# Optimization experiments

Measured on AMD Instinct MI355X. Metric: run time of the kernel, lower is better.

## Reference

```python
import jax, jax.numpy as jnp
import numpy as np

B, S, HID = 1, 2048, 2048
NH, NKV, HD = 32, 8, 64
SCALE = HD ** -0.5


def _rotary_tables(seq_len, dim, base=10000.0):
    inv_freq = 1.0 / (base ** (jnp.arange(0, dim, 2, dtype=jnp.float32) / dim))
    t = jnp.arange(seq_len, dtype=jnp.float32)
    freqs = jnp.outer(t, inv_freq)                      # [S, D/2]
    emb = jnp.concatenate([freqs, freqs], axis=-1)      # [S, D]
    return jnp.cos(emb)[None], jnp.sin(emb)[None]       # [1, S, D]


def setup_inputs() -> dict:
    key = jax.random.key(0)
    ks = jax.random.split(key, 5)
    cos, sin = _rotary_tables(S, HD)
    std = HID ** -0.5
    return {
        "hidden_states": jax.random.normal(ks[0], (B, S, HID), jnp.float32),
        "cos": cos,
        "sin": sin,
        "Wq": jax.random.normal(ks[1], (HID, NH * HD), jnp.float32) * std,
        "Wk": jax.random.normal(ks[2], (HID, NKV * HD), jnp.float32) * std,
        "Wv": jax.random.normal(ks[3], (HID, NKV * HD), jnp.float32) * std,
        "Wo": jax.random.normal(ks[4], (NH * HD, HID), jnp.float32) * std,
    }


def _rotate_half(x):
    x1, x2 = jnp.split(x, 2, axis=-1)
    return jnp.concatenate([-x2, x1], axis=-1)


def reference(hidden_states, cos, sin, Wq, Wk, Wv, Wo):
    b, s, _ = hidden_states.shape
    # projections -> [B, H, S, D]
    q = (hidden_states @ Wq).reshape(b, s, NH, HD).transpose(0, 2, 1, 3)
    k = (hidden_states @ Wk).reshape(b, s, NKV, HD).transpose(0, 2, 1, 3)
    v = (hidden_states @ Wv).reshape(b, s, NKV, HD).transpose(0, 2, 1, 3)
    # rotary embedding (broadcast over heads)
    c = cos[:, None, :, :]
    sn = sin[:, None, :, :]
    q = q * c + _rotate_half(q) * sn
    k = k * c + _rotate_half(k) * sn
    # GQA: repeat kv heads
    groups = NH // NKV
    k = jnp.repeat(k, groups, axis=1)
    v = jnp.repeat(v, groups, axis=1)
    scores = jnp.einsum("bhqd,bhkd->bhqk", q, k) * SCALE
    causal = jnp.tril(jnp.ones((s, s), dtype=bool))
    scores = jnp.where(causal, scores, jnp.finfo(scores.dtype).min)
    weights = jax.nn.softmax(scores, axis=-1)
    attn = jnp.einsum("bhqk,bhkd->bhqd", weights, v)
    attn = attn.transpose(0, 2, 1, 3).reshape(b, s, NH * HD)
    out = attn @ Wo
    return out, weights
```

## Files before the change

kernel.cpp:

```cpp
#include <hip/hip_runtime.h>

typedef short short8 __attribute__((ext_vector_type(8)));
typedef float f32x4 __attribute__((ext_vector_type(4)));

#define S_LEN 2048
#define HID 2048
#define NH 32
#define NKV 8
#define HD 64
#define DQKV 3072
#define SCALE 0.125f
#define SM_OFF 8.0f

static __device__ __forceinline__ unsigned short f2bf(float f) {
    unsigned int u = __float_as_uint(f);
    u += 0x7FFF + ((u >> 16) & 1);
    return (unsigned short)(u >> 16);
}
static __device__ __forceinline__ float bf2f(unsigned short u) {
    return __uint_as_float((unsigned int)u << 16);
}

#define GLDS16(g, l)                                                                     \
    __builtin_amdgcn_global_load_lds((const __attribute__((address_space(1))) unsigned int*)(g), \
                                     (__attribute__((address_space(3))) unsigned int*)(l), 16, 0, 0)

__global__ void prep(const float* __restrict__ Wq, const float* __restrict__ Wk,
                     const float* __restrict__ Wv, const float* __restrict__ Wo,
                     const float* __restrict__ hidden,
                     unsigned short* __restrict__ Wt, unsigned short* __restrict__ Wot,
                     unsigned short* __restrict__ Hb) {
    const int z = blockIdx.z;
    const int t = threadIdx.x;
    if (z == 4) {
        int idx = (blockIdx.y * 64 + blockIdx.x) * 256 + t;
        float4 v = ((const float4*)hidden)[idx];
        ushort4 o = {f2bf(v.x), f2bf(v.y), f2bf(v.z), f2bf(v.w)};
        ((ushort4*)Hb)[idx] = o;
        return;
    }
    const float* src; unsigned short* dst; int sld;
    if (z == 0)      { src = Wq; dst = Wt; sld = HID; }
    else if (z == 1) { if (blockIdx.x >= 16) return; src = Wk; dst = Wt + (size_t)2048 * HID; sld = 512; }
    else if (z == 2) { if (blockIdx.x >= 16) return; src = Wv; dst = Wt + (size_t)2560 * HID; sld = 512; }
    else             { src = Wo; dst = Wot; sld = HID; }
    __shared__ float tile[32][33];
    const int tx = t & 31, ty = t >> 5;
    const int r0 = blockIdx.y * 32, c0 = blockIdx.x * 32;
#pragma unroll
    for (int i = 0; i < 4; ++i)
        tile[ty * 4 + i][tx] = src[(size_t)(r0 + ty * 4 + i) * sld + c0 + tx];
    __syncthreads();
#pragma unroll
    for (int i = 0; i < 4; ++i)
        dst[(size_t)(c0 + ty * 4 + i) * HID + r0 + tx] = f2bf(tile[tx][ty * 4 + i]);
}

template <int MODE>
__global__ __launch_bounds__(512) void gemm_fused(const unsigned short* __restrict__ A,
                                                  const unsigned short* __restrict__ Bt,
                                                  float* __restrict__ C,
                                                  const float* __restrict__ cosb,
                                                  const float* __restrict__ sinb,
                                                  unsigned short* __restrict__ Qb,
                                                  unsigned short* __restrict__ Kb,
                                                  unsigned short* __restrict__ Vt,
                                                  int K, int lda, int ldb, int ldc) {
    __shared__ __align__(16) unsigned short As[128 * 64];
    __shared__ __align__(16) unsigned short Bs[128 * 64];
    const int t = threadIdx.x, lane = t & 63, wv = t >> 6;
    const int m0 = blockIdx.y * 128, n0 = blockIdx.x * 128;
    const int wm = wv >> 1, wn = wv & 1;
    const int lr = lane & 15, lg = lane >> 4;
    const int srow = lane >> 3;
    const int scol = ((lane & 7) ^ srow) * 8;
    f32x4 acc[2][4] = {};
    for (int k0 = 0; k0 < K; k0 += 64) {
        __syncthreads();
#pragma unroll
        for (int p = 0; p < 2; ++p) {
            int rbase = wv * 16 + p * 8;
            GLDS16(&A[(size_t)(m0 + rbase + srow) * lda + k0 + scol], &As[rbase * 64]);
            GLDS16(&Bt[(size_t)(n0 + rbase + srow) * ldb + k0 + scol], &Bs[rbase * 64]);
        }
        __syncthreads();
#pragma unroll
        for (int kk = 0; kk < 2; ++kk) {
            short8 a[2], b[4];
#pragma unroll
            for (int i = 0; i < 2; ++i) {
                int row = wm * 32 + i * 16 + lr;
                a[i] = *(const short8*)&As[row * 64 + (((kk * 4 + lg) ^ (row & 7)) * 8)];
            }
#pragma unroll
            for (int j = 0; j < 4; ++j) {
                int row = wn * 64 + j * 16 + lr;
                b[j] = *(const short8*)&Bs[row * 64 + (((kk * 4 + lg) ^ (row & 7)) * 8)];
            }
#pragma unroll
            for (int i = 0; i < 2; ++i)
#pragma unroll
                for (int j = 0; j < 4; ++j)
                    acc[i][j] = __builtin_amdgcn_mfma_f32_16x16x32_bf16(a[i], b[j], acc[i][j], 0, 0, 0);
        }
    }

    if (MODE == 1) {
#pragma unroll
        for (int i = 0; i < 2; ++i)
#pragma unroll
            for (int j = 0; j < 4; ++j)
#pragma unroll
                for (int r = 0; r < 4; ++r)
                    C[(size_t)(m0 + wm * 32 + i * 16 + lg * 4 + r) * ldc +
                      n0 + wn * 64 + j * 16 + lr] = acc[i][j][r];
        return;
    }

    const int head = (n0 + wn * 64) >> 6;
    if (head < NH + NKV) {
        unsigned short* dst = (head < NH) ? Qb : Kb;
        const int dld = (head < NH) ? HID : 512;
        const int hc = (head < NH) ? head * HD : (head - NH) * HD;
#pragma unroll
        for (int i = 0; i < 2; ++i) {
            const int s0 = m0 + wm * 32 + i * 16 + lg * 4;
#pragma unroll
            for (int j = 0; j < 2; ++j) {
                const int c = j * 16 + lr;
#pragma unroll
                for (int r = 0; r < 4; ++r) {
                    const int s = s0 + r;
                    float x1 = acc[i][j][r], x2 = acc[i][j + 2][r];
                    float c1 = cosb[s * HD + c],      s1 = sinb[s * HD + c];
                    float c2 = cosb[s * HD + c + 32], s2 = sinb[s * HD + c + 32];
                    dst[(size_t)s * dld + hc + c]      = f2bf(x1 * c1 - x2 * s1);
                    dst[(size_t)s * dld + hc + c + 32] = f2bf(x2 * c2 + x1 * s2);
                }
            }
        }
    } else {
        const int vh = head - NH - NKV;
#pragma unroll
        for (int i = 0; i < 2; ++i) {
            const int s0 = m0 + wm * 32 + i * 16 + lg * 4;
#pragma unroll
            for (int j = 0; j < 4; ++j) {
                const int d = vh * HD + j * 16 + lr;
                ushort4 o = {f2bf(acc[i][j][0]), f2bf(acc[i][j][1]),
                             f2bf(acc[i][j][2]), f2bf(acc[i][j][3])};
                *(ushort4*)&Vt[(size_t)d * S_LEN + s0] = o;
            }
        }
    }
}

#define KSZ (128 * 72)
#define VSZ (64 * 136)
__global__ __launch_bounds__(512) void attn_fused(const unsigned short* __restrict__ Qb,
                                                  const unsigned short* __restrict__ Kb,
                                                  const unsigned short* __restrict__ Vt,
                                                  float* __restrict__ w,
                                                  unsigned short* __restrict__ Ab) {
    __shared__ __align__(16) unsigned short Ks[2 * KSZ];
    __shared__ __align__(16) unsigned short Vs[2 * VSZ];
    __shared__ __align__(16) unsigned short Ps[8][32 * 40];
    const int p = blockIdx.x, h = blockIdx.y, kvh = h >> 2;
    const int t = threadIdx.x, lane = t & 63, wv = t >> 6;
    const int grp = wv & 1, wr = wv >> 1;
    const int qt = grp ? (15 - p) : p;
    const int q0 = qt * 128;
    const int lr = lane & 15, lg = lane >> 4;
    const int ktmax = 15 - p;
    unsigned short* Pw = &Ps[wv][0];

    const float C1 = SCALE;
    const float NEG = -1.0e30f;

    short8 qf[2][2];
#pragma unroll
    for (int i = 0; i < 2; ++i)
#pragma unroll
        for (int kk = 0; kk < 2; ++kk)
            qf[i][kk] = *(const short8*)&Qb[(size_t)(q0 + wr * 32 + i * 16 + lr) * HID +
                                            h * HD + kk * 32 + lg * 8];

    const int krow = t >> 2, kc = (t & 3) * 16;
    const int vrow = t >> 3, vc = (t & 7) * 16;

    short8 kA, kB, vA, vB;
#define LOADK(kt) { const unsigned short* kp = &Kb[(size_t)((kt) * 128 + krow) * 512 + kvh * HD]; \
                    kA = *(const short8*)&kp[kc]; kB = *(const short8*)&kp[kc + 8]; }
#define WRITEK(b) { *(short8*)&Ks[(b) * KSZ + krow * 72 + kc] = kA;                 \
                    *(short8*)&Ks[(b) * KSZ + krow * 72 + kc + 8] = kB; }
#define LOADV(kt) { const unsigned short* vp = &Vt[(size_t)(kvh * HD + vrow) * S_LEN + (kt) * 128]; \
                    vA = *(const short8*)&vp[vc]; vB = *(const short8*)&vp[vc + 8]; }
#define WRITEV(b) { *(short8*)&Vs[(b) * VSZ + vrow * 136 + vc] = vA;                \
                    *(short8*)&Vs[(b) * VSZ + vrow * 136 + vc + 8] = vB; }
#define ZEROTILE(kt) {                                                              \
        f32x4 z4 = {0.f, 0.f, 0.f, 0.f};                                            \
        for (int rr = 0; rr < 16; ++rr) {                                           \
            int row = wr * 32 + rr * 2 + (lane >> 5);                               \
            *(f32x4*)&w[((size_t)h * S_LEN + q0 + row) * S_LEN + (kt) * 128 + (lane & 31) * 4] = z4; \
        }                                                                           \
    }

    float l_r[2] = {0.f, 0.f};

    LOADK(0); WRITEK(0);
    __syncthreads();
    LOADK(1);
    for (int kt = 0; kt <= ktmax; ++kt) {
        const int b = kt & 1;
        if (kt <= qt) {
            f32x4 acc[8][2] = {};
            __builtin_amdgcn_s_setprio(1);
#pragma unroll
            for (int kk = 0; kk < 2; ++kk) {
                short8 af[8];
#pragma unroll
                for (int j = 0; j < 8; ++j)
                    af[j] = *(const short8*)&Ks[b * KSZ + (j * 16 + lr) * 72 + kk * 32 + lg * 8];
#pragma unroll
                for (int j = 0; j < 8; ++j)
#pragma unroll
                    for (int i = 0; i < 2; ++i)
                        acc[j][i] = __builtin_amdgcn_mfma_f32_16x16x32_bf16(af[j], qf[i][kk], acc[j][i], 0, 0, 0);
            }
            __builtin_amdgcn_s_setprio(0);
            if (kt == qt) {
#pragma unroll
                for (int i = 0; i < 2; ++i) {
                    const int qg = q0 + wr * 32 + i * 16 + lr;
                    float sum = 0.f;
#pragma unroll
                    for (int j = 0; j < 8; ++j)
#pragma unroll
                        for (int r = 0; r < 4; ++r) {
                            int kg = kt * 128 + j * 16 + lg * 4 + r;
                            float s2 = fmaf(acc[j][i][r], C1, -SM_OFF);
                            s2 = (kg <= qg) ? s2 : NEG;
                            sum += __expf(s2);
                        }
                    sum += __shfl_xor(sum, 16);
                    sum += __shfl_xor(sum, 32);
                    l_r[i] += sum;
                }
            } else {
#pragma unroll
                for (int i = 0; i < 2; ++i) {
                    float sum = 0.f;
#pragma unroll
                    for (int j = 0; j < 8; ++j)
#pragma unroll
                        for (int r = 0; r < 4; ++r)
                            sum += __expf(fmaf(acc[j][i][r], C1, -SM_OFF));
                    sum += __shfl_xor(sum, 16);
                    sum += __shfl_xor(sum, 32);
                    l_r[i] += sum;
                }
            }
        } else {
            ZEROTILE(kt);
        }
        if (kt < ktmax) WRITEK(b ^ 1);
        __syncthreads();
        if (kt + 2 <= ktmax) LOADK(kt + 2);
    }
    for (int kt = ktmax + 1; kt < 16; ++kt) ZEROTILE(kt);

    const float invl[2] = {1.f / l_r[0], 1.f / l_r[1]};

    f32x4 o[2][4] = {};
    LOADK(0); LOADV(0); WRITEK(0); WRITEV(0);
    __syncthreads();
    LOADK(1); LOADV(1);
    for (int kt = 0; kt <= ktmax; ++kt) {
        const int b = kt & 1;
        if (kt <= qt) {
            f32x4 acc[8][2] = {};
            __builtin_amdgcn_s_setprio(1);
#pragma unroll
            for (int kk = 0; kk < 2; ++kk) {
                short8 af[8];
#pragma unroll
                for (int j = 0; j < 8; ++j)
                    af[j] = *(const short8*)&Ks[b * KSZ + (j * 16 + lr) * 72 + kk * 32 + lg * 8];
#pragma unroll
                for (int j = 0; j < 8; ++j)
#pragma unroll
                    for (int i = 0; i < 2; ++i)
                        acc[j][i] = __builtin_amdgcn_mfma_f32_16x16x32_bf16(af[j], qf[i][kk], acc[j][i], 0, 0, 0);
            }
            __builtin_amdgcn_s_setprio(0);
            const bool diag = (kt == qt);
#pragma unroll
            for (int ks = 0; ks < 4; ++ks) {
                if (diag) {
#pragma unroll
                    for (int i = 0; i < 2; ++i) {
                        const int qg = q0 + wr * 32 + i * 16 + lr;
#pragma unroll
                        for (int jj = 0; jj < 2; ++jj) {
                            const int j = ks * 2 + jj;
                            ushort4 pk;
#pragma unroll
                            for (int r = 0; r < 4; ++r) {
                                int kg = kt * 128 + j * 16 + lg * 4 + r;
                                float s2 = fmaf(acc[j][i][r], C1, -SM_OFF);
                                s2 = (kg <= qg) ? s2 : NEG;
                                ((unsigned short*)&pk)[r] = f2bf(__expf(s2) * invl[i]);
                            }
                            *(ushort4*)&Pw[(i * 16 + lr) * 40 + jj * 16 + lg * 4] = pk;
                        }
                    }
                } else {
#pragma unroll
                    for (int i = 0; i < 2; ++i)
#pragma unroll
                        for (int jj = 0; jj < 2; ++jj) {
                            const int j = ks * 2 + jj;
                            ushort4 pk;
#pragma unroll
                            for (int r = 0; r < 4; ++r)
                                ((unsigned short*)&pk)[r] =
                                    f2bf(__expf(fmaf(acc[j][i][r], C1, -SM_OFF)) * invl[i]);
                            *(ushort4*)&Pw[(i * 16 + lr) * 40 + jj * 16 + lg * 4] = pk;
                        }
                }
                short8 pa[2], vb[4];
#pragma unroll
                for (int i = 0; i < 2; ++i)
                    pa[i] = *(const short8*)&Pw[(i * 16 + lr) * 40 + lg * 8];
#pragma unroll
                for (int j2 = 0; j2 < 4; ++j2)
                    vb[j2] = *(const short8*)&Vs[b * VSZ + (j2 * 16 + lr) * 136 + ks * 32 + lg * 8];
                __builtin_amdgcn_s_setprio(1);
#pragma unroll
                for (int i = 0; i < 2; ++i)
#pragma unroll
                    for (int j2 = 0; j2 < 4; ++j2)
                        o[i][j2] = __builtin_amdgcn_mfma_f32_16x16x32_bf16(pa[i], vb[j2], o[i][j2], 0, 0, 0);
                __builtin_amdgcn_s_setprio(0);
#pragma unroll
                for (int rp = 0; rp < 2; ++rp) {
                    int rq = (lane >> 2) + rp * 16;
                    int cb = (lane & 3) * 8;
                    short8 pv8 = *(const short8*)&Pw[rq * 40 + cb];
                    f32x4 f0 = {bf2f((unsigned short)pv8[0]), bf2f((unsigned short)pv8[1]),
                                bf2f((unsigned short)pv8[2]), bf2f((unsigned short)pv8[3])};
                    f32x4 f1 = {bf2f((unsigned short)pv8[4]), bf2f((unsigned short)pv8[5]),
                                bf2f((unsigned short)pv8[6]), bf2f((unsigned short)pv8[7])};
                    size_t base = ((size_t)h * S_LEN + q0 + wr * 32 + rq) * S_LEN + kt * 128 + ks * 32 + cb;
                    *(f32x4*)&w[base] = f0;
                    *(f32x4*)&w[base + 4] = f1;
                }
            }
        }
        if (kt < ktmax) { WRITEK(b ^ 1); WRITEV(b ^ 1); }
        __syncthreads();
        if (kt + 2 <= ktmax) { LOADK(kt + 2); LOADV(kt + 2); }
    }
#pragma unroll
    for (int i = 0; i < 2; ++i)
#pragma unroll
        for (int j2 = 0; j2 < 4; ++j2)
#pragma unroll
            for (int r = 0; r < 4; ++r)
                Ab[(size_t)(q0 + wr * 32 + i * 16 + lg * 4 + r) * HID +
                   h * HD + j2 * 16 + lr] = f2bf(o[i][j2][r]);
}

extern "C" void kernel_launch(void* const* d_in, const int* in_sizes, int n_in,
                              void* d_out, int out_size, void* d_ws, size_t ws_size,
                              hipStream_t stream) {
    const float* hidden = (const float*)d_in[0];
    const float* cosb   = (const float*)d_in[1];
    const float* sinb   = (const float*)d_in[2];
    const float* Wq     = (const float*)d_in[3];
    const float* Wk     = (const float*)d_in[4];
    const float* Wv     = (const float*)d_in[5];
    const float* Wo     = (const float*)d_in[6];

    float* out_mat = (float*)d_out;
    float* weights = (float*)d_out + (size_t)S_LEN * HID;

    char* wsb = (char*)d_ws;
    unsigned short* Hb  = (unsigned short*)wsb;
    unsigned short* Wt  = (unsigned short*)(wsb + (size_t)8  * 1024 * 1024);
    unsigned short* Wot = (unsigned short*)(wsb + (size_t)20 * 1024 * 1024);
    unsigned short* Qb  = (unsigned short*)(wsb + (size_t)28 * 1024 * 1024);
    unsigned short* Kb  = (unsigned short*)(wsb + (size_t)36 * 1024 * 1024);
    unsigned short* Vt  = (unsigned short*)(wsb + (size_t)38 * 1024 * 1024);
    unsigned short* Ab  = (unsigned short*)(wsb + (size_t)40 * 1024 * 1024);

    prep<<<dim3(64, 64, 5), 256, 0, stream>>>(Wq, Wk, Wv, Wo, hidden, Wt, Wot, Hb);

    gemm_fused<0><<<dim3(DQKV / 128, S_LEN / 128), 512, 0, stream>>>(
        Hb, Wt, nullptr, cosb, sinb, Qb, Kb, Vt, HID, HID, HID, 0);

    attn_fused<<<dim3(8, NH), 512, 0, stream>>>(Qb, Kb, Vt, weights, Ab);

    gemm_fused<1><<<dim3(HID / 128, S_LEN / 128), 512, 0, stream>>>(
        Ab, Wot, out_mat, nullptr, nullptr, nullptr, nullptr, nullptr, HID, HID, HID, HID);
}
```

Measured before the change: 247.8 us.

## Split attention blocks to one query tile each, single-buffer LDS

The attention kernel previously paired two complementary query tiles (p and 15-p) in one 512-thread block to balance causal work. It now launches 16x32 blocks of 256 threads, each handling a single query tile, largest first. K/V staging drops to a single LDS buffer with a two-barrier load/write/compute pattern, and the s_setprio hints are removed. This cuts LDS per block and allows more blocks per CU, but loses the built-in load balancing and the double-buffered overlap of global loads with MFMA work.

After: 254.1 us. +2.6%, slower.

```diff
diff --git a/kernel.cpp b/kernel.cpp
--- a/kernel.cpp
+++ b/kernel.cpp
@@ -155,23 +155,18 @@
     }
 }
 
-#define KSZ (128 * 72)
-#define VSZ (64 * 136)
-__global__ __launch_bounds__(512) void attn_fused(const unsigned short* __restrict__ Qb,
+__global__ __launch_bounds__(256) void attn_fused(const unsigned short* __restrict__ Qb,
                                                   const unsigned short* __restrict__ Kb,
                                                   const unsigned short* __restrict__ Vt,
                                                   float* __restrict__ w,
                                                   unsigned short* __restrict__ Ab) {
-    __shared__ __align__(16) unsigned short Ks[2 * KSZ];
-    __shared__ __align__(16) unsigned short Vs[2 * VSZ];
-    __shared__ __align__(16) unsigned short Ps[8][32 * 40];
-    const int p = blockIdx.x, h = blockIdx.y, kvh = h >> 2;
+    __shared__ __align__(16) unsigned short Ks[128 * 72];
+    __shared__ __align__(16) unsigned short Vs[64 * 136];
+    __shared__ __align__(16) unsigned short Ps[4][32 * 40];
+    const int qt = 15 - blockIdx.x, h = blockIdx.y, kvh = h >> 2;
     const int t = threadIdx.x, lane = t & 63, wv = t >> 6;
-    const int grp = wv & 1, wr = wv >> 1;
-    const int qt = grp ? (15 - p) : p;
     const int q0 = qt * 128;
     const int lr = lane & 15, lg = lane >> 4;
-    const int ktmax = 15 - p;
     unsigned short* Pw = &Ps[wv][0];
 
     const float C1 = SCALE;
@@ -182,184 +177,173 @@
     for (int i = 0; i < 2; ++i)
 #pragma unroll
         for (int kk = 0; kk < 2; ++kk)
-            qf[i][kk] = *(const short8*)&Qb[(size_t)(q0 + wr * 32 + i * 16 + lr) * HID +
+            qf[i][kk] = *(const short8*)&Qb[(size_t)(q0 + wv * 32 + i * 16 + lr) * HID +
                                             h * HD + kk * 32 + lg * 8];
 
-    const int krow = t >> 2, kc = (t & 3) * 16;
-    const int vrow = t >> 3, vc = (t & 7) * 16;
-
-    short8 kA, kB, vA, vB;
-#define LOADK(kt) { const unsigned short* kp = &Kb[(size_t)((kt) * 128 + krow) * 512 + kvh * HD]; \
-                    kA = *(const short8*)&kp[kc]; kB = *(const short8*)&kp[kc + 8]; }
-#define WRITEK(b) { *(short8*)&Ks[(b) * KSZ + krow * 72 + kc] = kA;                 \
-                    *(short8*)&Ks[(b) * KSZ + krow * 72 + kc + 8] = kB; }
-#define LOADV(kt) { const unsigned short* vp = &Vt[(size_t)(kvh * HD + vrow) * S_LEN + (kt) * 128]; \
-                    vA = *(const short8*)&vp[vc]; vB = *(const short8*)&vp[vc + 8]; }
-#define WRITEV(b) { *(short8*)&Vs[(b) * VSZ + vrow * 136 + vc] = vA;                \
-                    *(short8*)&Vs[(b) * VSZ + vrow * 136 + vc + 8] = vB; }
+    const int kr0 = t >> 2, kc = (t & 3) * 16;
+    const int vr0 = t >> 2, vc = (t & 3) * 16;
+
+    short8 kA, kB, kC, kD, vA, vB, vC, vD;
+#define LOADK(kt) { const unsigned short* kp = &Kb[(size_t)((kt) * 128 + kr0) * 512 + kvh * HD]; \
+                    kA = *(const short8*)&kp[kc]; kB = *(const short8*)&kp[kc + 8];              \
+                    const unsigned short* kq = kp + 64 * 512;                                    \
+                    kC = *(const short8*)&kq[kc]; kD = *(const short8*)&kq[kc + 8]; }
+#define WRITEK()  { *(short8*)&Ks[kr0 * 72 + kc] = kA; *(short8*)&Ks[kr0 * 72 + kc + 8] = kB;   \
+                    *(short8*)&Ks[(kr0 + 64) * 72 + kc] = kC;                                    \
+                    *(short8*)&Ks[(kr0 + 64) * 72 + kc + 8] = kD; }
+#define LOADV(kt) { const unsigned short* vp = &Vt[(size_t)(kvh * HD + vr0) * S_LEN + (kt) * 128]; \
+                    vA = *(const short8*)&vp[vc]; vB = *(const short8*)&vp[vc + 8];              \
+                    vC = *(const short8*)&vp[vc + 64]; vD = *(const short8*)&vp[vc + 72]; }
+#define WRITEV()  { *(short8*)&Vs[vr0 * 136 + vc] = vA; *(short8*)&Vs[vr0 * 136 + vc + 8] = vB; \
+                    *(short8*)&Vs[vr0 * 136 + vc + 64] = vC;                                     \
+                    *(short8*)&Vs[vr0 * 136 + vc + 72] = vD; }
 #define ZEROTILE(kt) {                                                              \
         f32x4 z4 = {0.f, 0.f, 0.f, 0.f};                                            \
         for (int rr = 0; rr < 16; ++rr) {                                           \
-            int row = wr * 32 + rr * 2 + (lane >> 5);                               \
+            int row = wv * 32 + rr * 2 + (lane >> 5);                               \
             *(f32x4*)&w[((size_t)h * S_LEN + q0 + row) * S_LEN + (kt) * 128 + (lane & 31) * 4] = z4; \
         }                                                                           \
     }
 
     float l_r[2] = {0.f, 0.f};
 
-    LOADK(0); WRITEK(0);
-    __syncthreads();
-    LOADK(1);
-    for (int kt = 0; kt <= ktmax; ++kt) {
-        const int b = kt & 1;
-        if (kt <= qt) {
-            f32x4 acc[8][2] = {};
-            __builtin_amdgcn_s_setprio(1);
-#pragma unroll
-            for (int kk = 0; kk < 2; ++kk) {
-                short8 af[8];
+    LOADK(0);
+    for (int kt = 0; kt <= qt; ++kt) {
+        __syncthreads();
+        WRITEK();
+        __syncthreads();
+        if (kt < qt) LOADK(kt + 1);
+        f32x4 acc[8][2] = {};
+#pragma unroll
+        for (int kk = 0; kk < 2; ++kk) {
+            short8 af[8];
+#pragma unroll
+            for (int j = 0; j < 8; ++j)
+                af[j] = *(const short8*)&Ks[(j * 16 + lr) * 72 + kk * 32 + lg * 8];
+#pragma unroll
+            for (int j = 0; j < 8; ++j)
+#pragma unroll
+                for (int i = 0; i < 2; ++i)
+                    acc[j][i] = __builtin_amdgcn_mfma_f32_16x16x32_bf16(af[j], qf[i][kk], acc[j][i], 0, 0, 0);
+        }
+        if (kt == qt) {
+#pragma unroll
+            for (int i = 0; i < 2; ++i) {
+                const int qg = q0 + wv * 32 + i * 16 + lr;
+                float sum = 0.f;
 #pragma unroll
                 for (int j = 0; j < 8; ++j)
-                    af[j] = *(const short8*)&Ks[b * KSZ + (j * 16 + lr) * 72 + kk * 32 + lg * 8];
+#pragma unroll
+                    for (int r = 0; r < 4; ++r) {
+                        int kg = kt * 128 + j * 16 + lg * 4 + r;
+                        float s2 = fmaf(acc[j][i][r], C1, -SM_OFF);
+                        s2 = (kg <= qg) ? s2 : NEG;
+                        sum += __expf(s2);
+                    }
+                sum += __shfl_xor(sum, 16);
+                sum += __shfl_xor(sum, 32);
+                l_r[i] += sum;
+            }
+        } else {
+#pragma unroll
+            for (int i = 0; i < 2; ++i) {
+                float sum = 0.f;
 #pragma unroll
                 for (int j = 0; j < 8; ++j)
 #pragma unroll
-                    for (int i = 0; i < 2; ++i)
-                        acc[j][i] = __builtin_amdgcn_mfma_f32_16x16x32_bf16(af[j], qf[i][kk], acc[j][i], 0, 0, 0);
-            }
-            __builtin_amdgcn_s_setprio(0);
-            if (kt == qt) {
+                    for (int r = 0; r < 4; ++r)
+                        sum += __expf(fmaf(acc[j][i][r], C1, -SM_OFF));
+                sum += __shfl_xor(sum, 16);
+                sum += __shfl_xor(sum, 32);
+                l_r[i] += sum;
+            }
+        }
+    }
+    for (int kt = qt + 1; kt < 16; ++kt) ZEROTILE(kt);
+
+    const float invl[2] = {1.f / l_r[0], 1.f / l_r[1]};
+
+    f32x4 o[2][4] = {};
+    LOADK(0); LOADV(0);
+    for (int kt = 0; kt <= qt; ++kt) {
+        __syncthreads();
+        WRITEK(); WRITEV();
+        __syncthreads();
+        if (kt < qt) { LOADK(kt + 1); LOADV(kt + 1); }
+        f32x4 acc[8][2] = {};
+#pragma unroll
+        for (int kk = 0; kk < 2; ++kk) {
+            short8 af[8];
+#pragma unroll
+            for (int j = 0; j < 8; ++j)
+                af[j] = *(const short8*)&Ks[(j * 16 + lr) * 72 + kk * 32 + lg * 8];
+#pragma unroll
+            for (int j = 0; j < 8; ++j)
+#pragma unroll
+                for (int i = 0; i < 2; ++i)
+                    acc[j][i] = __builtin_amdgcn_mfma_f32_16x16x32_bf16(af[j], qf[i][kk], acc[j][i], 0, 0, 0);
+        }
+        const bool diag = (kt == qt);
+#pragma unroll
+        for (int ks = 0; ks < 4; ++ks) {
+            if (diag) {
 #pragma unroll
                 for (int i = 0; i < 2; ++i) {
-                    const int qg = q0 + wr * 32 + i * 16 + lr;
-                    float sum = 0.f;
-#pragma unroll
-                    for (int j = 0; j < 8; ++j)
+                    const int qg = q0 + wv * 32 + i * 16 + lr;
+#pragma unroll
+                    for (int jj = 0; jj < 2; ++jj) {
+                        const int j = ks * 2 + jj;
+                        ushort4 pk;
 #pragma unroll
                         for (int r = 0; r < 4; ++r) {
                             int kg = kt * 128 + j * 16 + lg * 4 + r;
                             float s2 = fmaf(acc[j][i][r], C1, -SM_OFF);
                             s2 = (kg <= qg) ? s2 : NEG;
-                            sum += __expf(s2);
+                            ((unsigned short*)&pk)[r] = f2bf(__expf(s2) * invl[i]);
                         }
-                    sum += __shfl_xor(sum, 16);
-                    sum += __shfl_xor(sum, 32);
-                    l_r[i] += sum;
+                        *(ushort4*)&Pw[(i * 16 + lr) * 40 + jj * 16 + lg * 4] = pk;
+                    }
                 }
             } else {
 #pragma unroll
-                for (int i = 0; i < 2; ++i) {
-                    float sum = 0.f;
-#pragma unroll
-                    for (int j = 0; j < 8; ++j)
+                for (int i = 0; i < 2; ++i)
+#pragma unroll
+                    for (int jj = 0; jj < 2; ++jj) {
+                        const int j = ks * 2 + jj;
+                        ushort4 pk;
 #pragma unroll
                         for (int r = 0; r < 4; ++r)
-                            sum += __expf(fmaf(acc[j][i][r], C1, -SM_OFF));
-                    sum += __shfl_xor(sum, 16);
-                    sum += __shfl_xor(sum, 32);
-                    l_r[i] += sum;
-                }
-            }
-        } else {
-            ZEROTILE(kt);
-        }
-        if (kt < ktmax) WRITEK(b ^ 1);
-        __syncthreads();
-        if (kt + 2 <= ktmax) LOADK(kt + 2);
-    }
-    for (int kt = ktmax + 1; kt < 16; ++kt) ZEROTILE(kt);
-
-    const float invl[2] = {1.f / l_r[0], 1.f / l_r[1]};
-
-    f32x4 o[2][4] = {};
-    LOADK(0); LOADV(0); WRITEK(0); WRITEV(0);
-    __syncthreads();
-    LOADK(1); LOADV(1);
-    for (int kt = 0; kt <= ktmax; ++kt) {
-        const int b = kt & 1;
-        if (kt <= qt) {
-            f32x4 acc[8][2] = {};
-            __builtin_amdgcn_s_setprio(1);
-#pragma unroll
-            for (int kk = 0; kk < 2; ++kk) {
-                short8 af[8];
-#pragma unroll
-                for (int j = 0; j < 8; ++j)
-                    af[j] = *(const short8*)&Ks[b * KSZ + (j * 16 + lr) * 72 + kk * 32 + lg * 8];
-#pragma unroll
-                for (int j = 0; j < 8; ++j)
-#pragma unroll
-                    for (int i = 0; i < 2; ++i)
-                        acc[j][i] = __builtin_amdgcn_mfma_f32_16x16x32_bf16(af[j], qf[i][kk], acc[j][i], 0, 0, 0);
-            }
-            __builtin_amdgcn_s_setprio(0);
-            const bool diag = (kt == qt);
-#pragma unroll
-            for (int ks = 0; ks < 4; ++ks) {
-                if (diag) {
-#pragma unroll
-                    for (int i = 0; i < 2; ++i) {
-                        const int qg = q0 + wr * 32 + i * 16 + lr;
-#pragma unroll
-                        for (int jj = 0; jj < 2; ++jj) {
-                            const int j = ks * 2 + jj;
-                            ushort4 pk;
-#pragma unroll
-                            for (int r = 0; r < 4; ++r) {
-                                int kg = kt * 128 + j * 16 + lg * 4 + r;
-                                float s2 = fmaf(acc[j][i][r], C1, -SM_OFF);
-                                s2 = (kg <= qg) ? s2 : NEG;
-                                ((unsigned short*)&pk)[r] = f2bf(__expf(s2) * invl[i]);
-                            }
-                            *(ushort4*)&Pw[(i * 16 + lr) * 40 + jj * 16 + lg * 4] = pk;
-                        }
+                            ((unsigned short*)&pk)[r] =
+                                f2bf(__expf(fmaf(acc[j][i][r], C1, -SM_OFF)) * invl[i]);
+                        *(ushort4*)&Pw[(i * 16 + lr) * 40 + jj * 16 + lg * 4] = pk;
                     }
-                } else {
-#pragma unroll
-                    for (int i = 0; i < 2; ++i)
-#pragma unroll
-                        for (int jj = 0; jj < 2; ++jj) {
-                            const int j = ks * 2 + jj;
-                            ushort4 pk;
-#pragma unroll
-                            for (int r = 0; r < 4; ++r)
-                                ((unsigned short*)&pk)[r] =
-                                    f2bf(__expf(fmaf(acc[j][i][r], C1, -SM_OFF)) * invl[i]);
-                            *(ushort4*)&Pw[(i * 16 + lr) * 40 + jj * 16 + lg * 4] = pk;
-                        }
-                }
-                short8 pa[2], vb[4];
-#pragma unroll
-                for (int i = 0; i < 2; ++i)
-                    pa[i] = *(const short8*)&Pw[(i * 16 + lr) * 40 + lg * 8];
+            }
+            short8 pa[2], vb[4];
+#pragma unroll
+            for (int i = 0; i < 2; ++i)
+                pa[i] = *(const short8*)&Pw[(i * 16 + lr) * 40 + lg * 8];
+#pragma unroll
+            for (int j2 = 0; j2 < 4; ++j2)
+                vb[j2] = *(const short8*)&Vs[(j2 * 16 + lr) * 136 + ks * 32 + lg * 8];
+#pragma unroll
+            for (int i = 0; i < 2; ++i)
 #pragma unroll
                 for (int j2 = 0; j2 < 4; ++j2)
-                    vb[j2] = *(const short8*)&Vs[b * VSZ + (j2 * 16 + lr) * 136 + ks * 32 + lg * 8];
-                __builtin_amdgcn_s_setprio(1);
-#pragma unroll
-                for (int i = 0; i < 2; ++i)
-#pragma unroll
-                    for (int j2 = 0; j2 < 4; ++j2)
-                        o[i][j2] = __builtin_amdgcn_mfma_f32_16x16x32_bf16(pa[i], vb[j2], o[i][j2], 0, 0, 0);
-                __builtin_amdgcn_s_setprio(0);
-#pragma unroll
-                for (int rp = 0; rp < 2; ++rp) {
-                    int rq = (lane >> 2) + rp * 16;
-                    int cb = (lane & 3) * 8;
-                    short8 pv8 = *(const short8*)&Pw[rq * 40 + cb];
-                    f32x4 f0 = {bf2f((unsigned short)pv8[0]), bf2f((unsigned short)pv8[1]),
-                                bf2f((unsigned short)pv8[2]), bf2f((unsigned short)pv8[3])};
-                    f32x4 f1 = {bf2f((unsigned short)pv8[4]), bf2f((unsigned short)pv8[5]),
-                                bf2f((unsigned short)pv8[6]), bf2f((unsigned short)pv8[7])};
-                    size_t base = ((size_t)h * S_LEN + q0 + wr * 32 + rq) * S_LEN + kt * 128 + ks * 32 + cb;
-                    *(f32x4*)&w[base] = f0;
-                    *(f32x4*)&w[base + 4] = f1;
-                }
-            }
-        }
-        if (kt < ktmax) { WRITEK(b ^ 1); WRITEV(b ^ 1); }
-        __syncthreads();
-        if (kt + 2 <= ktmax) { LOADK(kt + 2); LOADV(kt + 2); }
+                    o[i][j2] = __builtin_amdgcn_mfma_f32_16x16x32_bf16(pa[i], vb[j2], o[i][j2], 0, 0, 0);
+#pragma unroll
+            for (int rp = 0; rp < 2; ++rp) {
+                int rq = (lane >> 2) + rp * 16;
+                int cb = (lane & 3) * 8;
+                short8 pv8 = *(const short8*)&Pw[rq * 40 + cb];
+                f32x4 f0 = {bf2f((unsigned short)pv8[0]), bf2f((unsigned short)pv8[1]),
+                            bf2f((unsigned short)pv8[2]), bf2f((unsigned short)pv8[3])};
+                f32x4 f1 = {bf2f((unsigned short)pv8[4]), bf2f((unsigned short)pv8[5]),
+                            bf2f((unsigned short)pv8[6]), bf2f((unsigned short)pv8[7])};
+                size_t base = ((size_t)h * S_LEN + q0 + wv * 32 + rq) * S_LEN + kt * 128 + ks * 32 + cb;
+                *(f32x4*)&w[base] = f0;
+                *(f32x4*)&w[base + 4] = f1;
+            }
+        }
     }
 #pragma unroll
     for (int i = 0; i < 2; ++i)
@@ -367,7 +351,7 @@
         for (int j2 = 0; j2 < 4; ++j2)
 #pragma unroll
             for (int r = 0; r < 4; ++r)
-                Ab[(size_t)(q0 + wr * 32 + i * 16 + lg * 4 + r) * HID +
+                Ab[(size_t)(q0 + wv * 32 + i * 16 + lg * 4 + r) * HID +
                    h * HD + j2 * 16 + lr] = f2bf(o[i][j2][r]);
 }
 
@@ -399,7 +383,7 @@
     gemm_fused<0><<<dim3(DQKV / 128, S_LEN / 128), 512, 0, stream>>>(
         Hb, Wt, nullptr, cosb, sinb, Qb, Kb, Vt, HID, HID, HID, 0);
 
-    attn_fused<<<dim3(8, NH), 512, 0, stream>>>(Qb, Kb, Vt, weights, Ab);
+    attn_fused<<<dim3(16, NH), 256, 0, stream>>>(Qb, Kb, Vt, weights, Ab);
 
     gemm_fused<1><<<dim3(HID / 128, S_LEN / 128), 512, 0, stream>>>(
         Ab, Wot, out_mat, nullptr, nullptr, nullptr, nullptr, nullptr, HID, HID, HID, HID);
```
